# Kernel tuning notes

Measured on AMD Instinct MI355X. Metric: run time of the kernel, lower is better.

The kernel has to match this reference:

```python
import jax, jax.numpy as jnp
import numpy as np

B, D, H, STEPS = 32768, 8, 64, 100


def setup_inputs() -> dict:
    key = jax.random.key(0)
    ks = jax.random.split(key, 7)
    def lin(k, shape, fan_in):
        # torch nn.Linear default init: U(-1/sqrt(fan_in), 1/sqrt(fan_in))
        return jax.random.uniform(k, shape, jnp.float32, -1.0, 1.0) / np.sqrt(fan_in).astype(np.float32)
    return {
        "x0": jax.random.normal(ks[0], (B, D), jnp.float32),
        "W1": lin(ks[1], (H, D + 1), D + 1),
        "b1": lin(ks[2], (H,), D + 1),
        "W2": lin(ks[3], (H, H), H),
        "b2": lin(ks[4], (H,), H),
        "W3": lin(ks[5], (D, H), H),
        "b3": lin(ks[6], (D,), H),
        "num_steps": STEPS,
    }


def _mlp(x, t_col, W1, b1, W2, b2, W3, b3):
    # x: [B, D], t_col: [B, 1] -> dx/dt: [B, D]
    xt = jnp.concatenate([x, t_col], axis=1)          # [B, D+1]
    h = jnp.tanh(xt @ W1.T + b1)                      # [B, H]
    h = jnp.tanh(h @ W2.T + b2)                       # [B, H]
    return h @ W3.T + b3                              # [B, D]


def reference(x0, W1, b1, W2, b2, W3, b3, num_steps):
    t0, t1 = 0.0, 1.0
    dt = (t1 - t0) / num_steps
    n, d = x0.shape
    ones_out = jnp.ones((n, d), x0.dtype)

    def step(carry, i):
        x, ld = carry
        t_col = jnp.full((n, 1), t0, x0.dtype) + i.astype(x0.dtype) * dt
        dx = _mlp(x, t_col, W1, b1, W2, b2, W3, b3)
        x_new = x + dt * dx
        # Faithful to torch source: grad of dx_dt.sum() wrt x evaluated at the
        # POST-step x (this is J^T @ 1, then summed over input dims).
        f = lambda xx: _mlp(xx, t_col, W1, b1, W2, b2, W3, b3)
        _, vjp_fn = jax.vjp(f, x_new)
        (g,) = vjp_fn(ones_out)                       # [B, D]
        ld_new = ld + dt * g.sum(axis=1)
        return (x_new, ld_new), None

    init = (x0, jnp.zeros(n, x0.dtype))
    (x, log_det), _ = jax.lax.scan(step, init, jnp.arange(num_steps))
    return x, log_det
```

## Files before the change

### kernel.cpp

```cpp
#include <hip/hip_runtime.h>


#define TSCALE 2.885390081777926815f

__device__ __forceinline__ float frcp3(float z) {
    float e = __builtin_amdgcn_exp2f(z);
    return __builtin_amdgcn_rcpf(e + 1.0f);
}

typedef __attribute__((ext_vector_type(8))) _Float16 v8h;
typedef __attribute__((ext_vector_type(2))) __fp16 v2fp;
typedef __attribute__((ext_vector_type(4))) float v4f;
typedef __attribute__((ext_vector_type(2))) float v2f;

union FragU {
    v8h h;
    unsigned u[4];
};

__device__ __forceinline__ unsigned pk16(float a, float b) {
    v2fp t = __builtin_amdgcn_cvt_pkrtz(a, b);
    return __builtin_bit_cast(unsigned, t);
}
__device__ __forceinline__ unsigned pk16v(v2f v) { return pk16(v.x, v.y); }

__device__ __forceinline__ unsigned pksig(unsigned sp) {
    v2fp s = __builtin_bit_cast(v2fp, sp);
    v2fp r = s - s * s;
    return __builtin_bit_cast(unsigned, r);
}

__device__ __forceinline__ int physj(int ks, int q, int jj) {
    return 16 * (ks + 2 * (jj >> 2)) + 4 * q + (jj & 3);
}

__device__ __forceinline__ void rename(const uint2 ph[4], FragU bh[2]) {
#pragma unroll
    for (int ks = 0; ks < 2; ++ks) {
        bh[ks].u[0] = ph[ks].x;
        bh[ks].u[1] = ph[ks].y;
        bh[ks].u[2] = ph[ks + 2].x;
        bh[ks].u[3] = ph[ks + 2].y;
    }
}

__global__ __launch_bounds__(256, 2) void cnf_fused(
    const float* __restrict__ x0, const float* __restrict__ W1,
    const float* __restrict__ b1, const float* __restrict__ W2,
    const float* __restrict__ b2, const float* __restrict__ W3,
    const float* __restrict__ b3, const int* __restrict__ nsp,
    float* __restrict__ out, int rows) {
    const int tid = threadIdx.x;
    const int w = tid >> 6;
    const int lane = tid & 63;
    const int c = lane & 15;
    const int q = lane >> 4;
    const int row0 = blockIdx.x * 64 + w * 16;

    const int n = *nsp;
    const float dt = 1.0f / (float)n;

    FragU a1[4];
#pragma unroll
    for (int mt = 0; mt < 4; ++mt) {
        const int m = 16 * mt + c;
        float f[8] = {0.f, 0.f, 0.f, 0.f, 0.f, 0.f, 0.f, 0.f};
        if (q == 0) {
#pragma unroll
            for (int jj = 0; jj < 4; ++jj) f[jj] = TSCALE * W1[m * 9 + jj];
            f[4] = TSCALE * W1[m * 9 + 8];
            f[5] = TSCALE * b1[m];
        } else if (q == 1) {
#pragma unroll
            for (int jj = 0; jj < 4; ++jj) f[jj] = TSCALE * W1[m * 9 + 4 + jj];
        }
#pragma unroll
        for (int p = 0; p < 4; ++p) a1[mt].u[p] = pk16(f[2 * p], f[2 * p + 1]);
    }
    FragU a2[4][2], a2g[4][2], a2d[4][2];
#pragma unroll
    for (int mt = 0; mt < 4; ++mt) {
        const int m = 16 * mt + c;
        float w3cm = 0.f;
#pragma unroll
        for (int d = 0; d < 8; ++d) w3cm += W3[d * 64 + m];
#pragma unroll
        for (int ks = 0; ks < 2; ++ks) {
            float f[8], fg[8], fd[8];
#pragma unroll
            for (int jj = 0; jj < 8; ++jj) {
                const int pj = physj(ks, q, jj);
                const float wv = W2[m * 64 + pj];
                float w1r = 0.f;
#pragma unroll
                for (int k = 0; k < 8; ++k) w1r += W1[pj * 9 + k];
                f[jj] = -2.0f * TSCALE * wv;
                fg[jj] = 16.0f * w3cm * wv * w1r;
                fd[jj] = 8.0f * wv * (dt * W1[pj * 9 + 8]);
            }
#pragma unroll
            for (int p = 0; p < 4; ++p) {
                a2[mt][ks].u[p] = pk16(f[2 * p], f[2 * p + 1]);
                a2g[mt][ks].u[p] = pk16(fg[2 * p], fg[2 * p + 1]);
                a2d[mt][ks].u[p] = pk16(fd[2 * p], fd[2 * p + 1]);
            }
        }
    }
    FragU a3[2];
#pragma unroll
    for (int ks = 0; ks < 2; ++ks) {
        float f[8];
#pragma unroll
        for (int jj = 0; jj < 8; ++jj)
            f[jj] = -2.0f * W3[(c & 7) * 64 + physj(ks, q, jj)];
#pragma unroll
        for (int p = 0; p < 4; ++p) a3[ks].u[p] = pk16(f[2 * p], f[2 * p + 1]);
    }

    const v4f vzero = {0.f, 0.f, 0.f, 0.f};
    FragU ones;
    ones.u[0] = ones.u[1] = ones.u[2] = ones.u[3] = 0x3C003C00u;

    v4f vb2[4];
#pragma unroll
    for (int mt = 0; mt < 4; ++mt) {
        v4f t = __builtin_amdgcn_mfma_f32_16x16x32_f16(a2[mt][0].h, ones.h, vzero, 0, 0, 0);
        t = __builtin_amdgcn_mfma_f32_16x16x32_f16(a2[mt][1].h, ones.h, t, 0, 0, 0);
        const int j0 = 16 * mt + 4 * q;
#pragma unroll
        for (int r = 0; r < 4; ++r)
            vb2[mt][r] = TSCALE * b2[j0 + r] - 0.5f * t[r];
    }
    v4f vb3;
    {
        v4f t = __builtin_amdgcn_mfma_f32_16x16x32_f16(a3[0].h, ones.h, vzero, 0, 0, 0);
        t = __builtin_amdgcn_mfma_f32_16x16x32_f16(a3[1].h, ones.h, t, 0, 0, 0);
#pragma unroll
        for (int r = 0; r < 4; ++r) vb3[r] = b3[(4 * q + r) & 7] - 0.5f * t[r];
    }

    float xr[4];
    {
        float4 v = *(const float4*)(x0 + (size_t)(row0 + c) * 8 + 4 * (q & 1));
        xr[0] = v.x; xr[1] = v.y; xr[2] = v.z; xr[3] = v.w;
    }
    v2f gv = {0.f, 0.f};

    {
        FragU bx;
        bx.u[0] = pk16(xr[0], xr[1]);
        bx.u[1] = pk16(xr[2], xr[3]);
        bx.u[2] = pk16(0.0f, 1.0f);
        bx.u[3] = 0u;
        v4f d1[4];
#pragma unroll
        for (int mt = 0; mt < 4; ++mt)
            d1[mt] = __builtin_amdgcn_mfma_f32_16x16x32_f16(a1[mt].h, bx.h, vzero, 0, 0, 0);
        uint2 ps[4];
#pragma unroll
        for (int mt = 0; mt < 4; ++mt) {
            ps[mt].x = pk16(frcp3(d1[mt][0]), frcp3(d1[mt][1]));
            ps[mt].y = pk16(frcp3(d1[mt][2]), frcp3(d1[mt][3]));
        }
        FragU bs[2];
        rename(ps, bs);
        v4f d2[4];
#pragma unroll
        for (int mt = 0; mt < 4; ++mt) {
            d2[mt] = __builtin_amdgcn_mfma_f32_16x16x32_f16(a2[mt][0].h, bs[0].h, vb2[mt], 0, 0, 0);
            d2[mt] = __builtin_amdgcn_mfma_f32_16x16x32_f16(a2[mt][1].h, bs[1].h, d2[mt], 0, 0, 0);
        }
#pragma unroll
        for (int mt = 0; mt < 4; ++mt) {
            ps[mt].x = pk16(frcp3(d2[mt][0]), frcp3(d2[mt][1]));
            ps[mt].y = pk16(frcp3(d2[mt][2]), frcp3(d2[mt][3]));
        }
        FragU bs2[2];
        rename(ps, bs2);
        v4f d3;
        d3 = __builtin_amdgcn_mfma_f32_16x16x32_f16(a3[0].h, bs2[0].h, vb3, 0, 0, 0);
        d3 = __builtin_amdgcn_mfma_f32_16x16x32_f16(a3[1].h, bs2[1].h, d3, 0, 0, 0);
#pragma unroll
        for (int r = 0; r < 4; ++r) xr[r] = fmaf(dt, d3[r], xr[r]);
    }

    float tp = 0.0f;
    for (int i = 1; i < n; ++i) {
        FragU bx;
        bx.u[0] = pk16(xr[0], xr[1]);
        bx.u[1] = pk16(xr[2], xr[3]);
        bx.u[2] = pk16(tp, 1.0f);
        bx.u[3] = 0u;
        tp += dt;
        v4f d1[4];
#pragma unroll
        for (int mt = 0; mt < 4; ++mt)
            d1[mt] = __builtin_amdgcn_mfma_f32_16x16x32_f16(a1[mt].h, bx.h, vzero, 0, 0, 0);

        uint2 psb[4], psg[4];
#pragma unroll
        for (int mt = 0; mt < 4; ++mt) {
            psb[mt].x = pk16(frcp3(d1[mt][0]), frcp3(d1[mt][1]));
            psb[mt].y = pk16(frcp3(d1[mt][2]), frcp3(d1[mt][3]));
            psg[mt].x = pksig(psb[mt].x);
            psg[mt].y = pksig(psb[mt].y);
        }
        FragU bs[2], bo[2];
        rename(psb, bs);
        rename(psg, bo);

        v4f z2b[4], sg[4], dz2[4];
#pragma unroll
        for (int mt = 0; mt < 4; ++mt) {
            z2b[mt] = __builtin_amdgcn_mfma_f32_16x16x32_f16(a2[mt][0].h, bs[0].h, vb2[mt], 0, 0, 0);
            z2b[mt] = __builtin_amdgcn_mfma_f32_16x16x32_f16(a2[mt][1].h, bs[1].h, z2b[mt], 0, 0, 0);
            sg[mt] = __builtin_amdgcn_mfma_f32_16x16x32_f16(a2g[mt][0].h, bo[0].h, vzero, 0, 0, 0);
            sg[mt] = __builtin_amdgcn_mfma_f32_16x16x32_f16(a2g[mt][1].h, bo[1].h, sg[mt], 0, 0, 0);
            dz2[mt] = __builtin_amdgcn_mfma_f32_16x16x32_f16(a2d[mt][0].h, bo[0].h, vzero, 0, 0, 0);
            dz2[mt] = __builtin_amdgcn_mfma_f32_16x16x32_f16(a2d[mt][1].h, bo[1].h, dz2[mt], 0, 0, 0);
        }

        uint2 pu[4];
#pragma unroll
        for (int mt = 0; mt < 4; ++mt) {
            v2f s01 = {frcp3(z2b[mt][0]), frcp3(z2b[mt][1])};
            v2f s23 = {frcp3(z2b[mt][2]), frcp3(z2b[mt][3])};
            v2f g01 = s01 - s01 * s01;
            v2f g23 = s23 - s23 * s23;
            gv += g01 * v2f{sg[mt][0], sg[mt][1]};
            gv += g23 * v2f{sg[mt][2], sg[mt][3]};
            v2f u01 = s01 - g01 * v2f{dz2[mt][0], dz2[mt][1]};
            v2f u23 = s23 - g23 * v2f{dz2[mt][2], dz2[mt][3]};
            pu[mt].x = pk16v(u01);
            pu[mt].y = pk16v(u23);
        }
        FragU bu[2];
        rename(pu, bu);
        v4f d3;
        d3 = __builtin_amdgcn_mfma_f32_16x16x32_f16(a3[0].h, bu[0].h, vb3, 0, 0, 0);
        d3 = __builtin_amdgcn_mfma_f32_16x16x32_f16(a3[1].h, bu[1].h, d3, 0, 0, 0);
#pragma unroll
        for (int r = 0; r < 4; ++r) xr[r] = fmaf(dt, d3[r], xr[r]);
    }

    {
        FragU bx;
        bx.u[0] = pk16(xr[0], xr[1]);
        bx.u[1] = pk16(xr[2], xr[3]);
        bx.u[2] = pk16(tp, 1.0f);
        bx.u[3] = 0u;
        v4f d1[4];
#pragma unroll
        for (int mt = 0; mt < 4; ++mt)
            d1[mt] = __builtin_amdgcn_mfma_f32_16x16x32_f16(a1[mt].h, bx.h, vzero, 0, 0, 0);
        uint2 psb[4], psg[4];
#pragma unroll
        for (int mt = 0; mt < 4; ++mt) {
            psb[mt].x = pk16(frcp3(d1[mt][0]), frcp3(d1[mt][1]));
            psb[mt].y = pk16(frcp3(d1[mt][2]), frcp3(d1[mt][3]));
            psg[mt].x = pksig(psb[mt].x);
            psg[mt].y = pksig(psb[mt].y);
        }
        FragU bs[2], bo[2];
        rename(psb, bs);
        rename(psg, bo);
        v4f z2b[4], sg[4];
#pragma unroll
        for (int mt = 0; mt < 4; ++mt) {
            z2b[mt] = __builtin_amdgcn_mfma_f32_16x16x32_f16(a2[mt][0].h, bs[0].h, vb2[mt], 0, 0, 0);
            z2b[mt] = __builtin_amdgcn_mfma_f32_16x16x32_f16(a2[mt][1].h, bs[1].h, z2b[mt], 0, 0, 0);
            sg[mt] = __builtin_amdgcn_mfma_f32_16x16x32_f16(a2g[mt][0].h, bo[0].h, vzero, 0, 0, 0);
            sg[mt] = __builtin_amdgcn_mfma_f32_16x16x32_f16(a2g[mt][1].h, bo[1].h, sg[mt], 0, 0, 0);
        }
#pragma unroll
        for (int mt = 0; mt < 4; ++mt) {
            v2f s01 = {frcp3(z2b[mt][0]), frcp3(z2b[mt][1])};
            v2f s23 = {frcp3(z2b[mt][2]), frcp3(z2b[mt][3])};
            v2f g01 = s01 - s01 * s01;
            v2f g23 = s23 - s23 * s23;
            gv += g01 * v2f{sg[mt][0], sg[mt][1]};
            gv += g23 * v2f{sg[mt][2], sg[mt][3]};
        }
    }

    float g = gv.x + gv.y;
    g += __shfl_xor(g, 16);
    g += __shfl_xor(g, 32);
    if (q < 2) {
        float4 st = {xr[0], xr[1], xr[2], xr[3]};
        *(float4*)(out + (size_t)(row0 + c) * 8 + 4 * q) = st;
    }
    if (q == 0) out[(size_t)rows * 8 + row0 + c] = dt * g;
}

extern "C" void kernel_launch(void* const* d_in, const int* in_sizes, int n_in,
                              void* d_out, int out_size, void* d_ws, size_t ws_size,
                              hipStream_t stream) {
    const float* x0 = (const float*)d_in[0];
    const float* W1 = (const float*)d_in[1];
    const float* b1 = (const float*)d_in[2];
    const float* W2 = (const float*)d_in[3];
    const float* b2 = (const float*)d_in[4];
    const float* W3 = (const float*)d_in[5];
    const float* b3 = (const float*)d_in[6];
    const int* ns = (const int*)d_in[7];
    float* out = (float*)d_out;
    const int rows = in_sizes[0] / 8;

    hipLaunchKernelGGL(cnf_fused, dim3(rows / 64), dim3(256), 0, stream,
                       x0, W1, b1, W2, b2, W3, b3, ns, out, rows);
}
```

Before: 185.1 us.

## Defer log-det sg MFMA to next iteration to fill dependency stalls

```diff
diff --git a/kernel.cpp b/kernel.cpp
--- a/kernel.cpp
+++ b/kernel.cpp
@@ -184,6 +184,16 @@
         for (int r = 0; r < 4; ++r) xr[r] = fmaf(dt, d3[r], xr[r]);
     }
 
+    FragU boP[2];
+    boP[0].u[0] = boP[0].u[1] = boP[0].u[2] = boP[0].u[3] = 0u;
+    boP[1].u[0] = boP[1].u[1] = boP[1].u[2] = boP[1].u[3] = 0u;
+    v2f gp01[4], gp23[4];
+#pragma unroll
+    for (int mt = 0; mt < 4; ++mt) {
+        gp01[mt] = v2f{0.f, 0.f};
+        gp23[mt] = v2f{0.f, 0.f};
+    }
+
     float tp = 0.0f;
     for (int i = 1; i < n; ++i) {
         FragU bx;
@@ -197,6 +207,14 @@
         for (int mt = 0; mt < 4; ++mt)
             d1[mt] = __builtin_amdgcn_mfma_f32_16x16x32_f16(a1[mt].h, bx.h, vzero, 0, 0, 0);
 
+#pragma unroll
+        for (int mt = 0; mt < 4; ++mt) {
+            v4f sgp = __builtin_amdgcn_mfma_f32_16x16x32_f16(a2g[mt][0].h, boP[0].h, vzero, 0, 0, 0);
+            sgp = __builtin_amdgcn_mfma_f32_16x16x32_f16(a2g[mt][1].h, boP[1].h, sgp, 0, 0, 0);
+            gv += gp01[mt] * v2f{sgp[0], sgp[1]};
+            gv += gp23[mt] * v2f{sgp[2], sgp[3]};
+        }
+
         uint2 psb[4], psg[4];
 #pragma unroll
         for (int mt = 0; mt < 4; ++mt) {
@@ -205,19 +223,17 @@
             psg[mt].x = pksig(psb[mt].x);
             psg[mt].y = pksig(psb[mt].y);
         }
-        FragU bs[2], bo[2];
+        FragU bs[2];
         rename(psb, bs);
-        rename(psg, bo);
-
-        v4f z2b[4], sg[4], dz2[4];
+        rename(psg, boP);
+
+        v4f z2b[4], dz2[4];
 #pragma unroll
         for (int mt = 0; mt < 4; ++mt) {
             z2b[mt] = __builtin_amdgcn_mfma_f32_16x16x32_f16(a2[mt][0].h, bs[0].h, vb2[mt], 0, 0, 0);
             z2b[mt] = __builtin_amdgcn_mfma_f32_16x16x32_f16(a2[mt][1].h, bs[1].h, z2b[mt], 0, 0, 0);
-            sg[mt] = __builtin_amdgcn_mfma_f32_16x16x32_f16(a2g[mt][0].h, bo[0].h, vzero, 0, 0, 0);
-            sg[mt] = __builtin_amdgcn_mfma_f32_16x16x32_f16(a2g[mt][1].h, bo[1].h, sg[mt], 0, 0, 0);
-            dz2[mt] = __builtin_amdgcn_mfma_f32_16x16x32_f16(a2d[mt][0].h, bo[0].h, vzero, 0, 0, 0);
-            dz2[mt] = __builtin_amdgcn_mfma_f32_16x16x32_f16(a2d[mt][1].h, bo[1].h, dz2[mt], 0, 0, 0);
+            dz2[mt] = __builtin_amdgcn_mfma_f32_16x16x32_f16(a2d[mt][0].h, boP[0].h, vzero, 0, 0, 0);
+            dz2[mt] = __builtin_amdgcn_mfma_f32_16x16x32_f16(a2d[mt][1].h, boP[1].h, dz2[mt], 0, 0, 0);
         }
 
         uint2 pu[4];
@@ -227,8 +243,8 @@
             v2f s23 = {frcp3(z2b[mt][2]), frcp3(z2b[mt][3])};
             v2f g01 = s01 - s01 * s01;
             v2f g23 = s23 - s23 * s23;
-            gv += g01 * v2f{sg[mt][0], sg[mt][1]};
-            gv += g23 * v2f{sg[mt][2], sg[mt][3]};
+            gp01[mt] = g01;
+            gp23[mt] = g23;
             v2f u01 = s01 - g01 * v2f{dz2[mt][0], dz2[mt][1]};
             v2f u23 = s23 - g23 * v2f{dz2[mt][2], dz2[mt][3]};
             pu[mt].x = pk16v(u01);
@@ -241,6 +257,14 @@
         d3 = __builtin_amdgcn_mfma_f32_16x16x32_f16(a3[1].h, bu[1].h, d3, 0, 0, 0);
 #pragma unroll
         for (int r = 0; r < 4; ++r) xr[r] = fmaf(dt, d3[r], xr[r]);
+    }
+
+#pragma unroll
+    for (int mt = 0; mt < 4; ++mt) {
+        v4f sgp = __builtin_amdgcn_mfma_f32_16x16x32_f16(a2g[mt][0].h, boP[0].h, vzero, 0, 0, 0);
+        sgp = __builtin_amdgcn_mfma_f32_16x16x32_f16(a2g[mt][1].h, boP[1].h, sgp, 0, 0, 0);
+        gv += gp01[mt] * v2f{sgp[0], sgp[1]};
+        gv += gp23[mt] * v2f{sgp[2], sgp[3]};
     }
 
     {
```

Result: no change. 184.9 us (median of 2 runs) (-0.1%).

## Split hidden dimension across wave pairs with LDS exchange per step

Applied to the files above, without the earlier changes.

```diff
diff --git a/kernel.cpp b/kernel.cpp
--- a/kernel.cpp
+++ b/kernel.cpp
@@ -29,22 +29,29 @@
     v2fp r = s - s * s;
     return __builtin_bit_cast(unsigned, r);
 }
+__device__ __forceinline__ unsigned pmul16(unsigned a, unsigned b) {
+    v2fp x = __builtin_bit_cast(v2fp, a);
+    v2fp y = __builtin_bit_cast(v2fp, b);
+    v2fp r = x * y;
+    return __builtin_bit_cast(unsigned, r);
+}
 
 __device__ __forceinline__ int physj(int ks, int q, int jj) {
     return 16 * (ks + 2 * (jj >> 2)) + 4 * q + (jj & 3);
 }
 
-__device__ __forceinline__ void rename(const uint2 ph[4], FragU bh[2]) {
-#pragma unroll
-    for (int ks = 0; ks < 2; ++ks) {
-        bh[ks].u[0] = ph[ks].x;
-        bh[ks].u[1] = ph[ks].y;
-        bh[ks].u[2] = ph[ks + 2].x;
-        bh[ks].u[3] = ph[ks + 2].y;
-    }
-}
-
-__global__ __launch_bounds__(256, 2) void cnf_fused(
+__device__ __forceinline__ void asm4(int half, uint2 o0, uint2 o1, uint4 s,
+                                     uint2& p0, uint2& p1, uint2& p2, uint2& p3) {
+    if (half == 0) {
+        p0 = o0; p1 = o1;
+        p2 = uint2{s.x, s.y}; p3 = uint2{s.z, s.w};
+    } else {
+        p0 = uint2{s.x, s.y}; p1 = uint2{s.z, s.w};
+        p2 = o0; p3 = o1;
+    }
+}
+
+__global__ __launch_bounds__(256, 4) void cnf_fused(
     const float* __restrict__ x0, const float* __restrict__ W1,
     const float* __restrict__ b1, const float* __restrict__ W2,
     const float* __restrict__ b2, const float* __restrict__ W3,
@@ -55,15 +62,22 @@
     const int lane = tid & 63;
     const int c = lane & 15;
     const int q = lane >> 4;
-    const int row0 = blockIdx.x * 64 + w * 16;
+    const int pair = w >> 1;
+    const int half = w & 1;
+    const int mtb = 2 * half;
+    const int ws = w ^ 1;
+    const int row0 = blockIdx.x * 32 + pair * 16;
+
+    __shared__ unsigned ex1[4][64][8];
+    __shared__ float ex2[4][64][8];
 
     const int n = *nsp;
     const float dt = 1.0f / (float)n;
 
-    FragU a1[4];
-#pragma unroll
-    for (int mt = 0; mt < 4; ++mt) {
-        const int m = 16 * mt + c;
+    FragU a1h[2];
+#pragma unroll
+    for (int jmt = 0; jmt < 2; ++jmt) {
+        const int m = 16 * (mtb + jmt) + c;
         float f[8] = {0.f, 0.f, 0.f, 0.f, 0.f, 0.f, 0.f, 0.f};
         if (q == 0) {
 #pragma unroll
@@ -75,18 +89,18 @@
             for (int jj = 0; jj < 4; ++jj) f[jj] = TSCALE * W1[m * 9 + 4 + jj];
         }
 #pragma unroll
-        for (int p = 0; p < 4; ++p) a1[mt].u[p] = pk16(f[2 * p], f[2 * p + 1]);
-    }
-    FragU a2[4][2], a2g[4][2], a2d[4][2];
-#pragma unroll
-    for (int mt = 0; mt < 4; ++mt) {
-        const int m = 16 * mt + c;
+        for (int p = 0; p < 4; ++p) a1h[jmt].u[p] = pk16(f[2 * p], f[2 * p + 1]);
+    }
+    FragU a2h[2][2], a2gh[2][2];
+#pragma unroll
+    for (int jmt = 0; jmt < 2; ++jmt) {
+        const int m = 16 * (mtb + jmt) + c;
         float w3cm = 0.f;
 #pragma unroll
         for (int d = 0; d < 8; ++d) w3cm += W3[d * 64 + m];
 #pragma unroll
         for (int ks = 0; ks < 2; ++ks) {
-            float f[8], fg[8], fd[8];
+            float f[8], fg[8];
 #pragma unroll
             for (int jj = 0; jj < 8; ++jj) {
                 const int pj = physj(ks, q, jj);
@@ -96,47 +110,53 @@
                 for (int k = 0; k < 8; ++k) w1r += W1[pj * 9 + k];
                 f[jj] = -2.0f * TSCALE * wv;
                 fg[jj] = 16.0f * w3cm * wv * w1r;
-                fd[jj] = 8.0f * wv * (dt * W1[pj * 9 + 8]);
             }
 #pragma unroll
             for (int p = 0; p < 4; ++p) {
-                a2[mt][ks].u[p] = pk16(f[2 * p], f[2 * p + 1]);
-                a2g[mt][ks].u[p] = pk16(fg[2 * p], fg[2 * p + 1]);
-                a2d[mt][ks].u[p] = pk16(fd[2 * p], fd[2 * p + 1]);
+                a2h[jmt][ks].u[p] = pk16(f[2 * p], f[2 * p + 1]);
+                a2gh[jmt][ks].u[p] = pk16(fg[2 * p], fg[2 * p + 1]);
             }
         }
     }
-    FragU a3[2];
-#pragma unroll
-    for (int ks = 0; ks < 2; ++ks) {
+    uint2 cpkC[4];
+    {
+        const float cs = -4.0f * dt / TSCALE;
+#pragma unroll
+        for (int mt = 0; mt < 4; ++mt) {
+            const int j0 = 16 * mt + 4 * q;
+            cpkC[mt].x = pk16(cs * W1[j0 * 9 + 8], cs * W1[(j0 + 1) * 9 + 8]);
+            cpkC[mt].y = pk16(cs * W1[(j0 + 2) * 9 + 8], cs * W1[(j0 + 3) * 9 + 8]);
+        }
+    }
+    FragU a3h;
+    {
         float f[8];
 #pragma unroll
         for (int jj = 0; jj < 8; ++jj)
-            f[jj] = -2.0f * W3[(c & 7) * 64 + physj(ks, q, jj)];
-#pragma unroll
-        for (int p = 0; p < 4; ++p) a3[ks].u[p] = pk16(f[2 * p], f[2 * p + 1]);
+            f[jj] = -2.0f * W3[(c & 7) * 64 + 16 * (mtb + (jj >> 2)) + 4 * q + (jj & 3)];
+#pragma unroll
+        for (int p = 0; p < 4; ++p) a3h.u[p] = pk16(f[2 * p], f[2 * p + 1]);
     }
 
     const v4f vzero = {0.f, 0.f, 0.f, 0.f};
     FragU ones;
     ones.u[0] = ones.u[1] = ones.u[2] = ones.u[3] = 0x3C003C00u;
 
-    v4f vb2[4];
-#pragma unroll
-    for (int mt = 0; mt < 4; ++mt) {
-        v4f t = __builtin_amdgcn_mfma_f32_16x16x32_f16(a2[mt][0].h, ones.h, vzero, 0, 0, 0);
-        t = __builtin_amdgcn_mfma_f32_16x16x32_f16(a2[mt][1].h, ones.h, t, 0, 0, 0);
-        const int j0 = 16 * mt + 4 * q;
+    v4f vb2h[2];
+#pragma unroll
+    for (int jmt = 0; jmt < 2; ++jmt) {
+        v4f t = __builtin_amdgcn_mfma_f32_16x16x32_f16(a2h[jmt][0].h, ones.h, vzero, 0, 0, 0);
+        t = __builtin_amdgcn_mfma_f32_16x16x32_f16(a2h[jmt][1].h, ones.h, t, 0, 0, 0);
+        const int j0 = 16 * (mtb + jmt) + 4 * q;
+#pragma unroll
+        for (int r = 0; r < 4; ++r) vb2h[jmt][r] = TSCALE * b2[j0 + r] - 0.5f * t[r];
+    }
+    v4f vb3p;
+    {
+        v4f t = __builtin_amdgcn_mfma_f32_16x16x32_f16(a3h.h, ones.h, vzero, 0, 0, 0);
 #pragma unroll
         for (int r = 0; r < 4; ++r)
-            vb2[mt][r] = TSCALE * b2[j0 + r] - 0.5f * t[r];
-    }
-    v4f vb3;
-    {
-        v4f t = __builtin_amdgcn_mfma_f32_16x16x32_f16(a3[0].h, ones.h, vzero, 0, 0, 0);
-        t = __builtin_amdgcn_mfma_f32_16x16x32_f16(a3[1].h, ones.h, t, 0, 0, 0);
-#pragma unroll
-        for (int r = 0; r < 4; ++r) vb3[r] = b3[(4 * q + r) & 7] - 0.5f * t[r];
+            vb3p[r] = (half == 0 ? b3[(4 * q + r) & 7] : 0.0f) - 0.5f * t[r];
     }
 
     float xr[4];
@@ -152,36 +172,42 @@
         bx.u[1] = pk16(xr[2], xr[3]);
         bx.u[2] = pk16(0.0f, 1.0f);
         bx.u[3] = 0u;
-        v4f d1[4];
-#pragma unroll
-        for (int mt = 0; mt < 4; ++mt)
-            d1[mt] = __builtin_amdgcn_mfma_f32_16x16x32_f16(a1[mt].h, bx.h, vzero, 0, 0, 0);
-        uint2 ps[4];
-#pragma unroll
-        for (int mt = 0; mt < 4; ++mt) {
-            ps[mt].x = pk16(frcp3(d1[mt][0]), frcp3(d1[mt][1]));
-            ps[mt].y = pk16(frcp3(d1[mt][2]), frcp3(d1[mt][3]));
-        }
+        v4f d1h[2];
+#pragma unroll
+        for (int jmt = 0; jmt < 2; ++jmt)
+            d1h[jmt] = __builtin_amdgcn_mfma_f32_16x16x32_f16(a1h[jmt].h, bx.h, vzero, 0, 0, 0);
+        uint2 ob0, ob1;
+        ob0.x = pk16(frcp3(d1h[0][0]), frcp3(d1h[0][1]));
+        ob0.y = pk16(frcp3(d1h[0][2]), frcp3(d1h[0][3]));
+        ob1.x = pk16(frcp3(d1h[1][0]), frcp3(d1h[1][1]));
+        ob1.y = pk16(frcp3(d1h[1][2]), frcp3(d1h[1][3]));
+        *(uint4*)&ex1[w][lane][0] = uint4{ob0.x, ob0.y, ob1.x, ob1.y};
+        __syncthreads();
+        const uint4 ssb = *(const uint4*)&ex1[ws][lane][0];
+        uint2 p0, p1, p2, p3;
+        asm4(half, ob0, ob1, ssb, p0, p1, p2, p3);
         FragU bs[2];
-        rename(ps, bs);
-        v4f d2[4];
-#pragma unroll
-        for (int mt = 0; mt < 4; ++mt) {
-            d2[mt] = __builtin_amdgcn_mfma_f32_16x16x32_f16(a2[mt][0].h, bs[0].h, vb2[mt], 0, 0, 0);
-            d2[mt] = __builtin_amdgcn_mfma_f32_16x16x32_f16(a2[mt][1].h, bs[1].h, d2[mt], 0, 0, 0);
-        }
-#pragma unroll
-        for (int mt = 0; mt < 4; ++mt) {
-            ps[mt].x = pk16(frcp3(d2[mt][0]), frcp3(d2[mt][1]));
-            ps[mt].y = pk16(frcp3(d2[mt][2]), frcp3(d2[mt][3]));
-        }
-        FragU bs2[2];
-        rename(ps, bs2);
-        v4f d3;
-        d3 = __builtin_amdgcn_mfma_f32_16x16x32_f16(a3[0].h, bs2[0].h, vb3, 0, 0, 0);
-        d3 = __builtin_amdgcn_mfma_f32_16x16x32_f16(a3[1].h, bs2[1].h, d3, 0, 0, 0);
-#pragma unroll
-        for (int r = 0; r < 4; ++r) xr[r] = fmaf(dt, d3[r], xr[r]);
+        bs[0].u[0] = p0.x; bs[0].u[1] = p0.y; bs[0].u[2] = p2.x; bs[0].u[3] = p2.y;
+        bs[1].u[0] = p1.x; bs[1].u[1] = p1.y; bs[1].u[2] = p3.x; bs[1].u[3] = p3.y;
+        v4f z2h[2];
+#pragma unroll
+        for (int jmt = 0; jmt < 2; ++jmt) {
+            z2h[jmt] = __builtin_amdgcn_mfma_f32_16x16x32_f16(a2h[jmt][0].h, bs[0].h, vb2h[jmt], 0, 0, 0);
+            z2h[jmt] = __builtin_amdgcn_mfma_f32_16x16x32_f16(a2h[jmt][1].h, bs[1].h, z2h[jmt], 0, 0, 0);
+        }
+        FragU buo;
+        buo.u[0] = pk16(frcp3(z2h[0][0]), frcp3(z2h[0][1]));
+        buo.u[1] = pk16(frcp3(z2h[0][2]), frcp3(z2h[0][3]));
+        buo.u[2] = pk16(frcp3(z2h[1][0]), frcp3(z2h[1][1]));
+        buo.u[3] = pk16(frcp3(z2h[1][2]), frcp3(z2h[1][3]));
+        v4f d3p = __builtin_amdgcn_mfma_f32_16x16x32_f16(a3h.h, buo.h, vb3p, 0, 0, 0);
+        *(float4*)&ex2[w][lane][0] = float4{d3p[0], d3p[1], d3p[2], d3p[3]};
+        __syncthreads();
+        const float4 dss = *(const float4*)&ex2[ws][lane][0];
+        xr[0] = fmaf(dt, d3p[0] + dss.x, xr[0]);
+        xr[1] = fmaf(dt, d3p[1] + dss.y, xr[1]);
+        xr[2] = fmaf(dt, d3p[2] + dss.z, xr[2]);
+        xr[3] = fmaf(dt, d3p[3] + dss.w, xr[3]);
     }
 
     float tp = 0.0f;
@@ -192,55 +218,72 @@
         bx.u[2] = pk16(tp, 1.0f);
         bx.u[3] = 0u;
         tp += dt;
-        v4f d1[4];
-#pragma unroll
-        for (int mt = 0; mt < 4; ++mt)
-            d1[mt] = __builtin_amdgcn_mfma_f32_16x16x32_f16(a1[mt].h, bx.h, vzero, 0, 0, 0);
-
-        uint2 psb[4], psg[4];
-#pragma unroll
-        for (int mt = 0; mt < 4; ++mt) {
-            psb[mt].x = pk16(frcp3(d1[mt][0]), frcp3(d1[mt][1]));
-            psb[mt].y = pk16(frcp3(d1[mt][2]), frcp3(d1[mt][3]));
-            psg[mt].x = pksig(psb[mt].x);
-            psg[mt].y = pksig(psb[mt].y);
-        }
-        FragU bs[2], bo[2];
-        rename(psb, bs);
-        rename(psg, bo);
-
-        v4f z2b[4], sg[4], dz2[4];
-#pragma unroll
-        for (int mt = 0; mt < 4; ++mt) {
-            z2b[mt] = __builtin_amdgcn_mfma_f32_16x16x32_f16(a2[mt][0].h, bs[0].h, vb2[mt], 0, 0, 0);
-            z2b[mt] = __builtin_amdgcn_mfma_f32_16x16x32_f16(a2[mt][1].h, bs[1].h, z2b[mt], 0, 0, 0);
-            sg[mt] = __builtin_amdgcn_mfma_f32_16x16x32_f16(a2g[mt][0].h, bo[0].h, vzero, 0, 0, 0);
-            sg[mt] = __builtin_amdgcn_mfma_f32_16x16x32_f16(a2g[mt][1].h, bo[1].h, sg[mt], 0, 0, 0);
-            dz2[mt] = __builtin_amdgcn_mfma_f32_16x16x32_f16(a2d[mt][0].h, bo[0].h, vzero, 0, 0, 0);
-            dz2[mt] = __builtin_amdgcn_mfma_f32_16x16x32_f16(a2d[mt][1].h, bo[1].h, dz2[mt], 0, 0, 0);
-        }
-
-        uint2 pu[4];
-#pragma unroll
-        for (int mt = 0; mt < 4; ++mt) {
-            v2f s01 = {frcp3(z2b[mt][0]), frcp3(z2b[mt][1])};
-            v2f s23 = {frcp3(z2b[mt][2]), frcp3(z2b[mt][3])};
+        v4f d1h[2];
+#pragma unroll
+        for (int jmt = 0; jmt < 2; ++jmt)
+            d1h[jmt] = __builtin_amdgcn_mfma_f32_16x16x32_f16(a1h[jmt].h, bx.h, vzero, 0, 0, 0);
+
+        uint2 ob0, ob1, og0, og1;
+        ob0.x = pk16(frcp3(d1h[0][0]), frcp3(d1h[0][1]));
+        ob0.y = pk16(frcp3(d1h[0][2]), frcp3(d1h[0][3]));
+        ob1.x = pk16(frcp3(d1h[1][0]), frcp3(d1h[1][1]));
+        ob1.y = pk16(frcp3(d1h[1][2]), frcp3(d1h[1][3]));
+        og0.x = pksig(ob0.x); og0.y = pksig(ob0.y);
+        og1.x = pksig(ob1.x); og1.y = pksig(ob1.y);
+
+        *(uint4*)&ex1[w][lane][0] = uint4{ob0.x, ob0.y, ob1.x, ob1.y};
+        *(uint4*)&ex1[w][lane][4] = uint4{og0.x, og0.y, og1.x, og1.y};
+        __syncthreads();
+        const uint4 ssb = *(const uint4*)&ex1[ws][lane][0];
+        const uint4 ssg = *(const uint4*)&ex1[ws][lane][4];
+        uint2 pb0, pb1, pb2, pb3, pg0, pg1, pg2, pg3;
+        asm4(half, ob0, ob1, ssb, pb0, pb1, pb2, pb3);
+        asm4(half, og0, og1, ssg, pg0, pg1, pg2, pg3);
+        FragU bs[2], bo[2], bo2[2];
+        bs[0].u[0] = pb0.x; bs[0].u[1] = pb0.y; bs[0].u[2] = pb2.x; bs[0].u[3] = pb2.y;
+        bs[1].u[0] = pb1.x; bs[1].u[1] = pb1.y; bs[1].u[2] = pb3.x; bs[1].u[3] = pb3.y;
+        bo[0].u[0] = pg0.x; bo[0].u[1] = pg0.y; bo[0].u[2] = pg2.x; bo[0].u[3] = pg2.y;
+        bo[1].u[0] = pg1.x; bo[1].u[1] = pg1.y; bo[1].u[2] = pg3.x; bo[1].u[3] = pg3.y;
+        bo2[0].u[0] = pmul16(pg0.x, cpkC[0].x); bo2[0].u[1] = pmul16(pg0.y, cpkC[0].y);
+        bo2[0].u[2] = pmul16(pg2.x, cpkC[2].x); bo2[0].u[3] = pmul16(pg2.y, cpkC[2].y);
+        bo2[1].u[0] = pmul16(pg1.x, cpkC[1].x); bo2[1].u[1] = pmul16(pg1.y, cpkC[1].y);
+        bo2[1].u[2] = pmul16(pg3.x, cpkC[3].x); bo2[1].u[3] = pmul16(pg3.y, cpkC[3].y);
+
+        v4f z2bh[2], sgh[2], dz2h[2];
+#pragma unroll
+        for (int jmt = 0; jmt < 2; ++jmt) {
+            z2bh[jmt] = __builtin_amdgcn_mfma_f32_16x16x32_f16(a2h[jmt][0].h, bs[0].h, vb2h[jmt], 0, 0, 0);
+            z2bh[jmt] = __builtin_amdgcn_mfma_f32_16x16x32_f16(a2h[jmt][1].h, bs[1].h, z2bh[jmt], 0, 0, 0);
+            sgh[jmt] = __builtin_amdgcn_mfma_f32_16x16x32_f16(a2gh[jmt][0].h, bo[0].h, vzero, 0, 0, 0);
+            sgh[jmt] = __builtin_amdgcn_mfma_f32_16x16x32_f16(a2gh[jmt][1].h, bo[1].h, sgh[jmt], 0, 0, 0);
+            dz2h[jmt] = __builtin_amdgcn_mfma_f32_16x16x32_f16(a2h[jmt][0].h, bo2[0].h, vzero, 0, 0, 0);
+            dz2h[jmt] = __builtin_amdgcn_mfma_f32_16x16x32_f16(a2h[jmt][1].h, bo2[1].h, dz2h[jmt], 0, 0, 0);
+        }
+
+        uint2 pu[2];
+#pragma unroll
+        for (int jmt = 0; jmt < 2; ++jmt) {
+            v2f s01 = {frcp3(z2bh[jmt][0]), frcp3(z2bh[jmt][1])};
+            v2f s23 = {frcp3(z2bh[jmt][2]), frcp3(z2bh[jmt][3])};
             v2f g01 = s01 - s01 * s01;
             v2f g23 = s23 - s23 * s23;
-            gv += g01 * v2f{sg[mt][0], sg[mt][1]};
-            gv += g23 * v2f{sg[mt][2], sg[mt][3]};
-            v2f u01 = s01 - g01 * v2f{dz2[mt][0], dz2[mt][1]};
-            v2f u23 = s23 - g23 * v2f{dz2[mt][2], dz2[mt][3]};
-            pu[mt].x = pk16v(u01);
-            pu[mt].y = pk16v(u23);
-        }
-        FragU bu[2];
-        rename(pu, bu);
-        v4f d3;
-        d3 = __builtin_amdgcn_mfma_f32_16x16x32_f16(a3[0].h, bu[0].h, vb3, 0, 0, 0);
-        d3 = __builtin_amdgcn_mfma_f32_16x16x32_f16(a3[1].h, bu[1].h, d3, 0, 0, 0);
-#pragma unroll
-        for (int r = 0; r < 4; ++r) xr[r] = fmaf(dt, d3[r], xr[r]);
+            gv += g01 * v2f{sgh[jmt][0], sgh[jmt][1]};
+            gv += g23 * v2f{sgh[jmt][2], sgh[jmt][3]};
+            v2f u01 = s01 - g01 * v2f{dz2h[jmt][0], dz2h[jmt][1]};
+            v2f u23 = s23 - g23 * v2f{dz2h[jmt][2], dz2h[jmt][3]};
+            pu[jmt].x = pk16v(u01);
+            pu[jmt].y = pk16v(u23);
+        }
+        FragU buo;
+        buo.u[0] = pu[0].x; buo.u[1] = pu[0].y; buo.u[2] = pu[1].x; buo.u[3] = pu[1].y;
+        v4f d3p = __builtin_amdgcn_mfma_f32_16x16x32_f16(a3h.h, buo.h, vb3p, 0, 0, 0);
+        *(float4*)&ex2[w][lane][0] = float4{d3p[0], d3p[1], d3p[2], d3p[3]};
+        __syncthreads();
+        const float4 dss = *(const float4*)&ex2[ws][lane][0];
+        xr[0] = fmaf(dt, d3p[0] + dss.x, xr[0]);
+        xr[1] = fmaf(dt, d3p[1] + dss.y, xr[1]);
+        xr[2] = fmaf(dt, d3p[2] + dss.z, xr[2]);
+        xr[3] = fmaf(dt, d3p[3] + dss.w, xr[3]);
     }
 
     {
@@ -249,48 +292,60 @@
         bx.u[1] = pk16(xr[2], xr[3]);
         bx.u[2] = pk16(tp, 1.0f);
         bx.u[3] = 0u;
-        v4f d1[4];
-#pragma unroll
-        for (int mt = 0; mt < 4; ++mt)
-            d1[mt] = __builtin_amdgcn_mfma_f32_16x16x32_f16(a1[mt].h, bx.h, vzero, 0, 0, 0);
-        uint2 psb[4], psg[4];
-#pragma unroll
-        for (int mt = 0; mt < 4; ++mt) {
-            psb[mt].x = pk16(frcp3(d1[mt][0]), frcp3(d1[mt][1]));
-            psb[mt].y = pk16(frcp3(d1[mt][2]), frcp3(d1[mt][3]));
-            psg[mt].x = pksig(psb[mt].x);
-            psg[mt].y = pksig(psb[mt].y);
-        }
+        v4f d1h[2];
+#pragma unroll
+        for (int jmt = 0; jmt < 2; ++jmt)
+            d1h[jmt] = __builtin_amdgcn_mfma_f32_16x16x32_f16(a1h[jmt].h, bx.h, vzero, 0, 0, 0);
+        uint2 ob0, ob1, og0, og1;
+        ob0.x = pk16(frcp3(d1h[0][0]), frcp3(d1h[0][1]));
+        ob0.y = pk16(frcp3(d1h[0][2]), frcp3(d1h[0][3]));
+        ob1.x = pk16(frcp3(d1h[1][0]), frcp3(d1h[1][1]));
+        ob1.y = pk16(frcp3(d1h[1][2]), frcp3(d1h[1][3]));
+        og0.x = pksig(ob0.x); og0.y = pksig(ob0.y);
+        og1.x = pksig(ob1.x); og1.y = pksig(ob1.y);
+        *(uint4*)&ex1[w][lane][0] = uint4{ob0.x, ob0.y, ob1.x, ob1.y};
+        *(uint4*)&ex1[w][lane][4] = uint4{og0.x, og0.y, og1.x, og1.y};
+        __syncthreads();
+        const uint4 ssb = *(const uint4*)&ex1[ws][lane][0];
+        const uint4 ssg = *(const uint4*)&ex1[ws][lane][4];
+        uint2 pb0, pb1, pb2, pb3, pg0, pg1, pg2, pg3;
+        asm4(half, ob0, ob1, ssb, pb0, pb1, pb2, pb3);
+        asm4(half, og0, og1, ssg, pg0, pg1, pg2, pg3);
         FragU bs[2], bo[2];
-        rename(psb, bs);
-        rename(psg, bo);
-        v4f z2b[4], sg[4];
-#pragma unroll
-        for (int mt = 0; mt < 4; ++mt) {
-            z2b[mt] = __builtin_amdgcn_mfma_f32_16x16x32_f16(a2[mt][0].h, bs[0].h, vb2[mt], 0, 0, 0);
-            z2b[mt] = __builtin_amdgcn_mfma_f32_16x16x32_f16(a2[mt][1].h, bs[1].h, z2b[mt], 0, 0, 0);
-            sg[mt] = __builtin_amdgcn_mfma_f32_16x16x32_f16(a2g[mt][0].h, bo[0].h, vzero, 0, 0, 0);
-            sg[mt] = __builtin_amdgcn_mfma_f32_16x16x32_f16(a2g[mt][1].h, bo[1].h, sg[mt], 0, 0, 0);
-        }
-#pragma unroll
-        for (int mt = 0; mt < 4; ++mt) {
-            v2f s01 = {frcp3(z2b[mt][0]), frcp3(z2b[mt][1])};
-            v2f s23 = {frcp3(z2b[mt][2]), frcp3(z2b[mt][3])};
+        bs[0].u[0] = pb0.x; bs[0].u[1] = pb0.y; bs[0].u[2] = pb2.x; bs[0].u[3] = pb2.y;
+        bs[1].u[0] = pb1.x; bs[1].u[1] = pb1.y; bs[1].u[2] = pb3.x; bs[1].u[3] = pb3.y;
+        bo[0].u[0] = pg0.x; bo[0].u[1] = pg0.y; bo[0].u[2] = pg2.x; bo[0].u[3] = pg2.y;
+        bo[1].u[0] = pg1.x; bo[1].u[1] = pg1.y; bo[1].u[2] = pg3.x; bo[1].u[3] = pg3.y;
+        v4f z2bh[2], sgh[2];
+#pragma unroll
+        for (int jmt = 0; jmt < 2; ++jmt) {
+            z2bh[jmt] = __builtin_amdgcn_mfma_f32_16x16x32_f16(a2h[jmt][0].h, bs[0].h, vb2h[jmt], 0, 0, 0);
+            z2bh[jmt] = __builtin_amdgcn_mfma_f32_16x16x32_f16(a2h[jmt][1].h, bs[1].h, z2bh[jmt], 0, 0, 0);
+            sgh[jmt] = __builtin_amdgcn_mfma_f32_16x16x32_f16(a2gh[jmt][0].h, bo[0].h, vzero, 0, 0, 0);
+            sgh[jmt] = __builtin_amdgcn_mfma_f32_16x16x32_f16(a2gh[jmt][1].h, bo[1].h, sgh[jmt], 0, 0, 0);
+        }
+#pragma unroll
+        for (int jmt = 0; jmt < 2; ++jmt) {
+            v2f s01 = {frcp3(z2bh[jmt][0]), frcp3(z2bh[jmt][1])};
+            v2f s23 = {frcp3(z2bh[jmt][2]), frcp3(z2bh[jmt][3])};
             v2f g01 = s01 - s01 * s01;
             v2f g23 = s23 - s23 * s23;
-            gv += g01 * v2f{sg[mt][0], sg[mt][1]};
-            gv += g23 * v2f{sg[mt][2], sg[mt][3]};
+            gv += g01 * v2f{sgh[jmt][0], sgh[jmt][1]};
+            gv += g23 * v2f{sgh[jmt][2], sgh[jmt][3]};
         }
     }
 
     float g = gv.x + gv.y;
     g += __shfl_xor(g, 16);
     g += __shfl_xor(g, 32);
-    if (q < 2) {
+    ex2[w][lane][0] = g;
+    __syncthreads();
+    g += ex2[ws][lane][0];
+    if (half == 0 && q < 2) {
         float4 st = {xr[0], xr[1], xr[2], xr[3]};
         *(float4*)(out + (size_t)(row0 + c) * 8 + 4 * q) = st;
     }
-    if (q == 0) out[(size_t)rows * 8 + row0 + c] = dt * g;
+    if (half == 0 && q == 0) out[(size_t)rows * 8 + row0 + c] = dt * g;
 }
 
 extern "C" void kernel_launch(void* const* d_in, const int* in_sizes, int n_in,
@@ -307,6 +362,6 @@
     float* out = (float*)d_out;
     const int rows = in_sizes[0] / 8;
 
-    hipLaunchKernelGGL(cnf_fused, dim3(rows / 64), dim3(256), 0, stream,
+    hipLaunchKernelGGL(cnf_fused, dim3(rows / 32), dim3(256), 0, stream,
                        x0, W1, b1, W2, b2, W3, b3, ns, out, rows);
 }
```

New measurement: 259.6 us. +40.3%, slower.
